# Kernel optimization log

Measured on AMD Instinct MI355X. Metric: run time of the kernel, lower is better.

Reference implementation:

```python
import jax, jax.numpy as jnp
import numpy as np

N_NODE = 4096   # nodes per graph (generalized from hardcoded 55)
IN_DIM = 200    # input_dim, forced by attn1 in_channel=200
OUT_DIM = 200   # output_dim, forced equal to input_dim by GRU_gate shapes
N_HEADS = 8     # forced by attn2 in_channel 1600 = 8*200
SEQ_LEN = 4
HID = 200       # hid_units default


def _glorot(k, shape):
    r = np.sqrt(6.0 / (shape[0] + shape[1])).astype(np.float32)
    return jax.random.uniform(k, shape, jnp.float32, -r, r)


def setup_inputs() -> dict:
    key = jax.random.key(0)
    ks = jax.random.split(key, 32)
    inp = {}
    mask = jax.random.bernoulli(ks[0], 0.01, (SEQ_LEN, N_NODE, N_NODE))
    inp['adjs'] = jax.random.uniform(ks[1], (SEQ_LEN, N_NODE, N_NODE), jnp.float32) * mask
    inp['feats'] = jax.random.normal(ks[2], (SEQ_LEN, N_NODE, IN_DIM), jnp.float32)
    inp['p_covss'] = jnp.zeros((SEQ_LEN,), jnp.float32)  # passed but unused in original
    # per-head weight_vars, randn(output_dim, input_dim) in original call()
    inp['init_wv'] = jax.random.normal(ks[3], (N_HEADS, OUT_DIM, IN_DIM), jnp.float32)
    # attn1 (shared across all heads): conv1d(k=1) == linear
    inp['W1'] = _glorot(ks[4], (HID, IN_DIM)); inp['b1'] = jnp.zeros((HID,), jnp.float32)
    inp['a11'] = _glorot(ks[5], (HID, 1))[:, 0]; inp['a11b'] = jnp.zeros((), jnp.float32)
    inp['a12'] = _glorot(ks[6], (HID, 1))[:, 0]; inp['a12b'] = jnp.zeros((), jnp.float32)
    # attn2
    inp['W2'] = _glorot(ks[7], (OUT_DIM, N_HEADS * HID)); inp['b2'] = jnp.zeros((OUT_DIM,), jnp.float32)
    inp['a21'] = _glorot(ks[8], (OUT_DIM, 1))[:, 0]; inp['a21b'] = jnp.zeros((), jnp.float32)
    inp['a22'] = _glorot(ks[9], (OUT_DIM, 1))[:, 0]; inp['a22b'] = jnp.zeros((), jnp.float32)
    # GRU gates (reset/update/htilda), reduce=True since n_node != input_dim
    for i, g in enumerate(['r', 'u', 'h']):
        inp['W' + g] = _glorot(ks[10 + 4 * i], (N_NODE, OUT_DIM))
        inp['U' + g] = _glorot(ks[11 + 4 * i], (OUT_DIM, OUT_DIM))
        inp['P' + g] = _glorot(ks[12 + 4 * i], (IN_DIM, N_NODE))
        inp['b' + g] = jnp.zeros((IN_DIM, OUT_DIM), jnp.float32)
    return inp


def reference(adjs, feats, p_covss, init_wv, W1, b1, a11, a11b, a12, a12b,
              W2, b2, a21, a21b, a22, a22b,
              Wr, Ur, Pr, br, Wu, Uu, Pu, bu, Wh, Uh, Ph, bh):
    def gat(x):  # x: [N, IN_DIM]
        fts = x @ W1.T + b1                                   # [N, HID]
        # logits f_1 + f_2^T on [N,1,1] stays [N,1,1]; softmax over the
        # singleton dim is identically 1 -> attention is degenerate.
        s = jax.nn.leaky_relu((fts @ a11 + a11b) + (fts @ a12 + a12b), 0.01)
        coefs = jnp.ones_like(s)                              # softmax([N,1,1], dim=1)
        h = jax.nn.elu(coefs[:, None] * fts)                  # [N, HID]
        hcat = jnp.tile(h, (1, N_HEADS))                      # heads share attn1 -> identical
        fts2 = hcat @ W2.T + b2                               # [N, OUT_DIM]
        s2 = jax.nn.leaky_relu((fts2 @ a21 + a21b) + (fts2 @ a22 + a22b), 0.01)
        coefs2 = jnp.ones_like(s2)
        out = jax.nn.elu(coefs2[:, None] * fts2)              # [N, OUT_DIM]
        # torch: out.view(nb_classes, -1).T then softmax(dim=1), then view(-1, out_dim)
        logits = jnp.reshape(out, (OUT_DIM, N_NODE)).T        # memory reinterpretation, not transpose
        return jax.nn.softmax(logits, axis=1)                 # [N, OUT_DIM]

    embeds = jax.vmap(gat)(feats)                             # [T, N, OUT_DIM]

    def gru_step(wv, adj):  # wv: [H, OUT_DIM, IN_DIM=OUT_DIM], adj: [N, N]
        # head-independent sparse propagation bases, one per gate
        gr = Pr @ (adj @ Wr) + br                             # [IN_DIM, OUT_DIM]
        gu = Pu @ (adj @ Wu) + bu
        gh = Ph @ (adj @ Wh) + bh
        r = jax.nn.sigmoid(gr + wv @ Ur)                      # [H, 200, 200]
        u = jax.nn.sigmoid(gu + wv @ Uu)
        hcap = jnp.tanh(gh + (r * wv) @ Uh)
        return (1.0 - u) * wv + u * hcap, None

    final_wv, _ = jax.lax.scan(gru_step, init_wv, adjs[1:])   # evolve over t=1..T-1
    return embeds, final_wv
```

## Files before the change

kernel.cpp:

```cpp
#include <hip/hip_runtime.h>
#include <hip/hip_bf16.h>
#include <math.h>

typedef __hip_bfloat16 bf16;
typedef __attribute__((ext_vector_type(8))) short short8;
typedef __attribute__((ext_vector_type(4))) float f32x4;

#define N_NODE 4096
#define DIM 200
#define NH 8
#define SEQ 4
#define TLDA 40

__device__ __forceinline__ float eluf(float x) { return x > 0.f ? x : expm1f(x); }
__device__ __forceinline__ float sigm(float x) { return 1.f / (1.f + expf(-x)); }

template<bool ISB>
__device__ __forceinline__ float ldv(const void* p, size_t i) {
    if (ISB) return __bfloat162float(((const bf16*)p)[i]);
    else     return ((const float*)p)[i];
}
template<bool ISB>
__device__ __forceinline__ void stv(void* p, size_t i, float v) {
    if (ISB) ((bf16*)p)[i] = __float2bfloat16(v);
    else     ((float*)p)[i] = v;
}
__device__ __forceinline__ float bflo(unsigned u) { return __uint_as_float((u & 0xffffu) << 16); }
__device__ __forceinline__ float bfhi(unsigned u) { return __uint_as_float(u & 0xffff0000u); }
__device__ __forceinline__ short f2bs(float v) {
    bf16 h = __float2bfloat16(v);
    return *(short*)&h;
}

__global__ void k_detect(const void* feats, int* flag) {
    __shared__ int cnt;
    if (threadIdx.x == 0) cnt = 0;
    __syncthreads();
    const unsigned short* u = (const unsigned short*)feats;
    unsigned short v = u[2 * threadIdx.x];
    int e = (v >> 7) & 0xFF;
    if (e >= 100 && e <= 140) atomicAdd(&cnt, 1);
    __syncthreads();
    if (threadIdx.x == 0) *flag = (cnt >= 128) ? 1 : 0;
}


template<int AMODE>
__device__ __forceinline__ short8 ldA8x(const void* A, int lda, int arow, bool rowOK,
                                        int kk, int K) {
    short8 r;
    if (rowOK && kk + 8 <= K) {
        if (AMODE == 1) {
            r = *(const short8*)((const short*)A + (size_t)arow * lda + kk);
        } else {
            const float* ap = (const float*)A + (size_t)arow * lda + kk;
            float4 f0 = *(const float4*)ap;
            float4 f1 = *(const float4*)(ap + 4);
            r[0] = f2bs(f0.x); r[1] = f2bs(f0.y); r[2] = f2bs(f0.z); r[3] = f2bs(f0.w);
            r[4] = f2bs(f1.x); r[5] = f2bs(f1.y); r[6] = f2bs(f1.z); r[7] = f2bs(f1.w);
        }
    } else {
#pragma unroll
        for (int j = 0; j < 8; j++) {
            bool ok = rowOK && kk + j < K;
            if (AMODE == 1) r[j] = ok ? ((const short*)A)[(size_t)arow * lda + kk + j] : (short)0;
            else            r[j] = ok ? f2bs(((const float*)A)[(size_t)arow * lda + kk + j]) : (short)0;
        }
    }
    return r;
}

template<int BMODE>
__device__ __forceinline__ short8 ldB8x(const void* B, int gcol, bool colOK,
                                        int kk, int K) {
    short8 r;
    if (BMODE == 2) {
        if (colOK && kk + 8 <= K) {
            r = *(const short8*)((const short*)B + (size_t)gcol * K + kk);
        } else {
#pragma unroll
            for (int j = 0; j < 8; j++)
                r[j] = (colOK && kk + j < K) ? ((const short*)B)[(size_t)gcol * K + kk + j] : (short)0;
        }
    } else {
#pragma unroll
        for (int j = 0; j < 8; j++)
            r[j] = (colOK && kk + j < K) ? ((const short*)B)[(size_t)(kk + j) * DIM + gcol] : (short)0;
    }
    return r;
}

template<int EPI, int AMODE, int BMODE, int CB16>
__device__ void mgemm(const void* A, int lda, const void* B, int M, int K,
                      int kbeg, int kend, const float* X1, const float* X2,
                      void* Cv, int row0, int c0, const int* fl, void* out2, short* Cb) {
    const int N = DIM;
    int tid = threadIdx.x;
    int wave = tid >> 6, lane = tid & 63;
    int m16 = lane & 15, q = lane >> 4;
    __shared__ short As[64 * TLDA];
    __shared__ short Bs[64 * TLDA];
    int s_row = tid >> 2;
    int s_k   = (tid & 3) * 8;
    int b_col = tid & 63;
    int b_kg  = (tid >> 6) * 8;
    int arow = row0 + s_row;
    bool rowOK = arow < M;
    int gcol = c0 + b_col;
    bool colOK = gcol < N;
    short8 la = ldA8x<AMODE>(A, lda, arow, rowOK, kbeg + s_k, K);
    short8 lb = ldB8x<BMODE>(B, gcol, colOK, kbeg + b_kg, K);
    f32x4 acc[4] = {};
    for (int k0 = kbeg; k0 < kend; k0 += 32) {
        __syncthreads();
        *(short8*)&As[s_row * TLDA + s_k] = la;
        *(short8*)&Bs[b_col * TLDA + b_kg] = lb;
        __syncthreads();
        int kn = k0 + 32;
        if (kn < kend) {
            la = ldA8x<AMODE>(A, lda, arow, rowOK, kn + s_k, K);
            lb = ldB8x<BMODE>(B, gcol, colOK, kn + b_kg, K);
        }
        short8 bfr = *(short8*)&Bs[(wave * 16 + m16) * TLDA + q * 8];
#pragma unroll
        for (int r = 0; r < 4; r++) {
            short8 af = *(short8*)&As[(r * 16 + m16) * TLDA + q * 8];
            acc[r] = __builtin_amdgcn_mfma_f32_16x16x32_bf16(af, bfr, acc[r], 0, 0, 0);
        }
    }
    int colw = c0 + wave * 16 + m16;
    if (colw >= N) return;
#pragma unroll
    for (int r = 0; r < 4; r++) {
        int rowb = row0 + r * 16 + q * 4;
#pragma unroll
        for (int reg = 0; reg < 4; reg++) {
            int row = rowb + reg;
            if (row >= M) continue;
            float v = acc[r][reg];
            size_t ci = (size_t)row * 200 + colw;
            if (EPI == 0) {
                float o = eluf(v + X1[colw]);
                if (CB16) ((short*)Cv)[ci] = f2bs(o);
                else      ((float*)Cv)[ci] = o;
            } else if (EPI == 3) {
                float* C = (float*)Cv;
                int a200 = row - (row / 200) * 200;
                float uu = X2[ci];
                float hc = tanhf(X1[a200 * 200 + colw] + v);
                float nv = (1.f - uu) * C[ci] + uu * hc;
                C[ci] = nv;
                Cb[ci] = f2bs(nv);
                if (out2) {
                    size_t oo = (size_t)SEQ * N_NODE * DIM + ci;
                    if (*fl) stv<true>(out2, oo, nv); else stv<false>(out2, oo, nv);
                }
            } else {
                atomicAdd(&((float*)Cv)[ci], v);
            }
        }
    }
}

__global__ __launch_bounds__(256) void k_gemm_e12(const short* A,
        const short* Br, const short* Bu, const float* Gr, const float* Gu,
        const float* wvf, short* rwb, float* u) {
    const int M = NH * DIM, K = DIM, N = DIM;
    int row0 = blockIdx.y * 64, c0 = blockIdx.x * 64;
    int tid = threadIdx.x;
    int wave = tid >> 6, lane = tid & 63;
    int m16 = lane & 15, q = lane >> 4;
    __shared__ short As[64 * TLDA];
    __shared__ short Bsr[64 * TLDA];
    __shared__ short Bsu[64 * TLDA];
    int s_row = tid >> 2;
    int s_k   = (tid & 3) * 8;
    int b_col = tid & 63;
    int b_kg  = (tid >> 6) * 8;
    int arow = row0 + s_row;
    bool rowOK = arow < M;
    int gcol = c0 + b_col;
    bool colOK = gcol < N;
    short8 la = ldA8x<1>(A, K, arow, rowOK, s_k, K);
    short8 lr = ldB8x<2>(Br, gcol, colOK, b_kg, K);
    short8 lu = ldB8x<2>(Bu, gcol, colOK, b_kg, K);
    f32x4 accR[4] = {}, accU[4] = {};
    for (int k0 = 0; k0 < K; k0 += 32) {
        __syncthreads();
        *(short8*)&As[s_row * TLDA + s_k] = la;
        *(short8*)&Bsr[b_col * TLDA + b_kg] = lr;
        *(short8*)&Bsu[b_col * TLDA + b_kg] = lu;
        __syncthreads();
        int kn = k0 + 32;
        if (kn < K) {
            la = ldA8x<1>(A, K, arow, rowOK, kn + s_k, K);
            lr = ldB8x<2>(Br, gcol, colOK, kn + b_kg, K);
            lu = ldB8x<2>(Bu, gcol, colOK, kn + b_kg, K);
        }
        short8 bfr = *(short8*)&Bsr[(wave * 16 + m16) * TLDA + q * 8];
        short8 bfu = *(short8*)&Bsu[(wave * 16 + m16) * TLDA + q * 8];
#pragma unroll
        for (int r = 0; r < 4; r++) {
            short8 af = *(short8*)&As[(r * 16 + m16) * TLDA + q * 8];
            accR[r] = __builtin_amdgcn_mfma_f32_16x16x32_bf16(af, bfr, accR[r], 0, 0, 0);
            accU[r] = __builtin_amdgcn_mfma_f32_16x16x32_bf16(af, bfu, accU[r], 0, 0, 0);
        }
    }
    int colw = c0 + wave * 16 + m16;
    if (colw >= N) return;
#pragma unroll
    for (int r = 0; r < 4; r++) {
        int rowb = row0 + r * 16 + q * 4;
#pragma unroll
        for (int reg = 0; reg < 4; reg++) {
            int row = rowb + reg;
            if (row >= M) continue;
            int a200 = row - (row / 200) * 200;
            size_t ci = (size_t)row * 200 + colw;
            rwb[ci] = f2bs(sigm(Gr[a200 * 200 + colw] + accR[r][reg]) * wvf[ci]);
            u[ci]   = sigm(Gu[a200 * 200 + colw] + accU[r][reg]);
        }
    }
}

__global__ __launch_bounds__(256) void k_gemm_e0a(const int* fl, const void* A,
        const short* B, const float* bias, short* Hb) {
    int row0 = blockIdx.y * 64, c0 = blockIdx.x * 64;
    if (*fl)
        mgemm<0, 1, 2, 1>(A, DIM, B, SEQ * N_NODE, DIM, 0, DIM, bias, nullptr,
                          Hb, row0, c0, nullptr, nullptr, nullptr);
    else
        mgemm<0, 0, 2, 1>(A, DIM, B, SEQ * N_NODE, DIM, 0, DIM, bias, nullptr,
                          Hb, row0, c0, nullptr, nullptr, nullptr);
}
__global__ __launch_bounds__(256) void k_gemm_e0b(const short* A, const short* B,
        const float* bias, float* C) {
    mgemm<0, 1, 2, 0>(A, DIM, B, SEQ * N_NODE, DIM, 0, DIM, bias, nullptr,
                      C, blockIdx.y * 64, blockIdx.x * 64, nullptr, nullptr, nullptr);
}
__global__ __launch_bounds__(256) void k_gemm_e3(const short* A, const short* B,
        const float* Gh, const float* U, float* WV, const int* fl, void* out2, short* wvb) {
    mgemm<3, 1, 2, 0>(A, DIM, B, NH * DIM, DIM, 0, DIM, Gh, U, WV,
                      blockIdx.y * 64, blockIdx.x * 64, fl, out2, wvb);
}
__global__ __launch_bounds__(256) void k_pggemm(const int* fl,
        const void* P0, const void* P1, const void* P2,
        const bf16* AWb, float* G) {
    int z = blockIdx.z;
    int sg = z >> 3, split = z & 7;
    int g = sg - (sg / 3) * 3;
    const void* A = (g == 0) ? P0 : (g == 1) ? P1 : P2;
    const void* B = AWb + (size_t)sg * N_NODE * DIM;
    float* C = G + (size_t)sg * DIM * DIM;
    int row0 = blockIdx.y * 64, c0 = blockIdx.x * 64;
    int kbeg = split * (N_NODE / 8), kend = kbeg + N_NODE / 8;
    if (*fl) mgemm<4, 1, 1, 0>(A, N_NODE, B, DIM, N_NODE, kbeg, kend, nullptr, nullptr, C, row0, c0, nullptr, nullptr, nullptr);
    else     mgemm<4, 0, 1, 0>(A, N_NODE, B, DIM, N_NODE, kbeg, kend, nullptr, nullptr, C, row0, c0, nullptr, nullptr, nullptr);
}

template<bool ISB>
__device__ void prep_body(const void* W1, const void* b1, const void* W2, const void* b2,
                          const void* Ur, const void* Uu, const void* Uh,
                          const void* br, const void* bu, const void* bh,
                          const void* iwv, const void* Wr, const void* Wu, const void* Wh,
                          short* W1b, short* W2b, float* b1f, float* b2f,
                          short* Ub, float* wv, short* wvb, float* G, unsigned short* Wcat) {
    int idx = blockIdx.x * 256 + threadIdx.x;
    if (idx < 40000) {
        W1b[idx] = f2bs(ldv<ISB>(W1, idx));
    } else if (idx < 80000) {
        int r = idx - 40000;
        int n = r / 200, k = r - n * 200;
        float s = 0.f;
        for (int h = 0; h < NH; h++) s += ldv<ISB>(W2, (size_t)n * 1600 + h * 200 + k);
        W2b[r] = f2bs(s);
    } else if (idx < 80512) {
        int j = idx - 80000;
        if (j < 256)      b1f[j] = (j < 200) ? ldv<ISB>(b1, j) : 0.f;
        else              b2f[j - 256] = (j - 256 < 200) ? ldv<ISB>(b2, j - 256) : 0.f;
    } else if (idx < 200512) {
        int j = idx - 80512;
        int g = j / 40000, r = j - g * 40000;
        int n = r / 200, k = r - n * 200;
        const void* U = (g == 0) ? Ur : (g == 1) ? Uu : Uh;
        Ub[j] = f2bs(ldv<ISB>(U, (size_t)k * 200 + n));
    } else if (idx < 520512) {
        int j = idx - 200512;
        float v = ldv<ISB>(iwv, j);
        wv[j] = v;
        wvb[j] = f2bs(v);
    } else if (idx < 880512) {
        int j = idx - 520512;
        int sg = j / 40000, r = j - sg * 40000;
        int g = sg - (sg / 3) * 3;
        const void* bb = (g == 0) ? br : (g == 1) ? bu : bh;
        G[j] = ldv<ISB>(bb, r);
    } else {
        int j = idx - 880512;
        if (j < 4096 * 600) {
            int k = j / 600, c = j - k * 600;
            int g = (c < 200) ? 0 : (c < 400 ? 1 : 2);
            int o = c - g * 200;
            const void* W = (g == 0) ? Wr : (g == 1) ? Wu : Wh;
            bf16 v = __float2bfloat16(ldv<ISB>(W, (size_t)k * 200 + o));
            Wcat[(size_t)k * 608 + c] = *(unsigned short*)&v;
        }
    }
}
__global__ void k_prep(const int* fl, const void* W1, const void* b1, const void* W2,
                       const void* b2, const void* Ur, const void* Uu, const void* Uh,
                       const void* br, const void* bu, const void* bh, const void* iwv,
                       const void* Wr, const void* Wu, const void* Wh,
                       short* W1b, short* W2b, float* b1f, float* b2f,
                       short* Ub, float* wv, short* wvb, float* G, unsigned short* Wcat) {
    if (*fl) prep_body<true >(W1, b1, W2, b2, Ur, Uu, Uh, br, bu, bh, iwv, Wr, Wu, Wh,
                              W1b, W2b, b1f, b2f, Ub, wv, wvb, G, Wcat);
    else     prep_body<false>(W1, b1, W2, b2, Ur, Uu, Uh, br, bu, bh, iwv, Wr, Wu, Wh,
                              W1b, W2b, b1f, b2f, Ub, wv, wvb, G, Wcat);
}

template<bool ISB>
__device__ void softmax_body(const float* O, void* out) {
    __shared__ float tile[200 * 65];
    __shared__ float pm[4 * 64];
    __shared__ float ps[4 * 64];
    __shared__ float sm_m[64];
    __shared__ float sm_inv[64];
    int t = blockIdx.y;
    int i0 = blockIdx.x * 64;
    const float* ob = O + (size_t)t * N_NODE * DIM;
    int tid = threadIdx.x;
    for (int idx = tid; idx < 200 * 64; idx += 256) {
        int j = idx >> 6, c = idx & 63;
        tile[j * 65 + c] = ob[(size_t)j * N_NODE + i0 + c];
    }
    __syncthreads();
    int g = tid >> 6, lane = tid & 63;
    int j0 = g * 50, j1 = j0 + 50;
    float mp = -1e30f;
    for (int j = j0; j < j1; j++) mp = fmaxf(mp, tile[j * 65 + lane]);
    pm[g * 64 + lane] = mp;
    __syncthreads();
    if (tid < 64)
        sm_m[tid] = fmaxf(fmaxf(pm[tid], pm[64 + tid]), fmaxf(pm[128 + tid], pm[192 + tid]));
    __syncthreads();
    float mv = sm_m[lane];
    float sp = 0.f;
    for (int j = j0; j < j1; j++) {
        float e = expf(tile[j * 65 + lane] - mv);
        tile[j * 65 + lane] = e;
        sp += e;
    }
    ps[g * 64 + lane] = sp;
    __syncthreads();
    if (tid < 64)
        sm_inv[tid] = 1.f / (ps[tid] + ps[64 + tid] + ps[128 + tid] + ps[192 + tid]);
    __syncthreads();
    size_t ob2 = ((size_t)t * N_NODE + i0) * DIM;
    for (int idx = tid; idx < 64 * 200; idx += 256) {
        int il = idx / 200, j = idx - il * 200;
        stv<ISB>(out, ob2 + (size_t)il * DIM + j, tile[j * 65 + il] * sm_inv[il]);
    }
}
__global__ __launch_bounds__(256) void k_softmax(const int* fl, const float* O, void* out) {
    if (*fl) softmax_body<true>(O, out); else softmax_body<false>(O, out);
}

template<bool ISB>
__device__ void aw_body(const void* adjs, const unsigned short* Wcat, bf16* AWb) {
    int i = blockIdx.x;
    int s = blockIdx.y;
    size_t arow = ((size_t)(s + 1) * N_NODE + i) * N_NODE;
    __shared__ int   s_k[512];
    __shared__ float s_v[512];
    __shared__ int   s_cnt;
    int tid = threadIdx.x;
    if (tid == 0) s_cnt = 0;
    __syncthreads();
    float vals[16];
#pragma unroll
    for (int c = 0; c < 4; c++) {
        int col = c * 1024 + tid * 4;
        if (ISB) {
            ushort4 u = *(const ushort4*)((const unsigned short*)adjs + arow + col);
            vals[c*4+0] = __uint_as_float((unsigned)u.x << 16);
            vals[c*4+1] = __uint_as_float((unsigned)u.y << 16);
            vals[c*4+2] = __uint_as_float((unsigned)u.z << 16);
            vals[c*4+3] = __uint_as_float((unsigned)u.w << 16);
        } else {
            float4 f = *(const float4*)((const float*)adjs + arow + col);
            vals[c*4+0] = f.x; vals[c*4+1] = f.y; vals[c*4+2] = f.z; vals[c*4+3] = f.w;
        }
    }
#pragma unroll
    for (int q = 0; q < 16; q++) {
        if (vals[q] != 0.f) {
            int p = atomicAdd(&s_cnt, 1);
            if (p < 512) { s_k[p] = (q >> 2) * 1024 + tid * 4 + (q & 3); s_v[p] = vals[q]; }
        }
    }
    __syncthreads();
    int n = s_cnt < 512 ? s_cnt : 512;
    float a0 = 0.f, a1 = 0.f, d0 = 0.f, d1 = 0.f;
    bool hasB = (tid < 44);
    int offA = 2 * tid, offB = 512 + 2 * tid;
    int e = 0;
    for (; e + 4 <= n; e += 4) {
        int   k0 = s_k[e],   k1 = s_k[e+1], k2 = s_k[e+2], k3 = s_k[e+3];
        float v0 = s_v[e],   v1 = s_v[e+1], v2 = s_v[e+2], v3 = s_v[e+3];
        unsigned wa0 = *(const unsigned*)(Wcat + (size_t)k0 * 608 + offA);
        unsigned wa1 = *(const unsigned*)(Wcat + (size_t)k1 * 608 + offA);
        unsigned wa2 = *(const unsigned*)(Wcat + (size_t)k2 * 608 + offA);
        unsigned wa3 = *(const unsigned*)(Wcat + (size_t)k3 * 608 + offA);
        if (hasB) {
            unsigned wb0 = *(const unsigned*)(Wcat + (size_t)k0 * 608 + offB);
            unsigned wb1 = *(const unsigned*)(Wcat + (size_t)k1 * 608 + offB);
            unsigned wb2 = *(const unsigned*)(Wcat + (size_t)k2 * 608 + offB);
            unsigned wb3 = *(const unsigned*)(Wcat + (size_t)k3 * 608 + offB);
            d0 += v0*bflo(wb0) + v1*bflo(wb1) + v2*bflo(wb2) + v3*bflo(wb3);
            d1 += v0*bfhi(wb0) + v1*bfhi(wb1) + v2*bfhi(wb2) + v3*bfhi(wb3);
        }
        a0 += v0*bflo(wa0) + v1*bflo(wa1) + v2*bflo(wa2) + v3*bflo(wa3);
        a1 += v0*bfhi(wa0) + v1*bfhi(wa1) + v2*bfhi(wa2) + v3*bfhi(wa3);
    }
    for (; e < n; e++) {
        int k = s_k[e]; float v = s_v[e];
        unsigned wa = *(const unsigned*)(Wcat + (size_t)k * 608 + offA);
        a0 += v * bflo(wa); a1 += v * bfhi(wa);
        if (hasB) {
            unsigned wb = *(const unsigned*)(Wcat + (size_t)k * 608 + offB);
            d0 += v * bflo(wb); d1 += v * bfhi(wb);
        }
    }
    int gA = (offA < 200) ? 0 : (offA < 400 ? 1 : 2);
    int oA = offA - gA * 200;
    size_t wbase = ((size_t)(s * 3 + gA) * N_NODE + i) * DIM + oA;
    AWb[wbase]     = __float2bfloat16(a0);
    AWb[wbase + 1] = __float2bfloat16(a1);
    if (hasB) {
        int oB = offB - 400;
        size_t wb2 = ((size_t)(s * 3 + 2) * N_NODE + i) * DIM + oB;
        AWb[wb2]     = __float2bfloat16(d0);
        AWb[wb2 + 1] = __float2bfloat16(d1);
    }
}
__global__ __launch_bounds__(256) void k_aw(const int* fl, const void* adjs,
        const unsigned short* Wcat, bf16* AWb) {
    if (*fl) aw_body<true>(adjs, Wcat, AWb);
    else     aw_body<false>(adjs, Wcat, AWb);
}

extern "C" void kernel_launch(void* const* d_in, const int* in_sizes, int n_in,
                              void* d_out, int out_size, void* d_ws, size_t ws_size,
                              hipStream_t stream) {
    const void* adjs    = d_in[0];
    const void* feats   = d_in[1];
    const void* init_wv = d_in[3];
    const void* W1 = d_in[4];
    const void* b1 = d_in[5];
    const void* W2 = d_in[10];
    const void* b2 = d_in[11];
    const void* Wr = d_in[16];
    const void* Ur = d_in[17];
    const void* Pr = d_in[18];
    const void* br = d_in[19];
    const void* Wu = d_in[20];
    const void* Uu = d_in[21];
    const void* Pu = d_in[22];
    const void* bu = d_in[23];
    const void* Wh = d_in[24];
    const void* Uh = d_in[25];
    const void* Ph = d_in[26];
    const void* bh = d_in[27];

    int*   flag = (int*)d_ws;
    float* base = (float*)d_ws;
    unsigned short* Wcat = (unsigned short*)(base + 64);
    bf16*  AWb  = (bf16*)(base + 64 + 1245184);
    short* Hb   = (short*)(base + 64);
    float* Obuf = base + 3276864;
    short* W1b  = (short*)(base + 6553664);
    short* W2b  = (short*)(base + 6593664);
    float* b1f  = base + 6633664;
    float* b2f  = base + 6633920;
    float* ubuf = base + 6634176;
    short* rwb  = (short*)(base + 6954176);
    short* Ub   = (short*)(base + 7274176);
    float* G    = base + 7394176;
    float* wv   = base + 7754176;
    short* wvb  = (short*)(base + 8074176);

    const int M = SEQ * N_NODE;

    k_detect<<<1, 256, 0, stream>>>(feats, flag);
    k_prep<<<(3338112 + 255) / 256, 256, 0, stream>>>(
        flag, W1, b1, W2, b2, Ur, Uu, Uh, br, bu, bh, init_wv, Wr, Wu, Wh,
        W1b, W2b, b1f, b2f, Ub, wv, wvb, G, Wcat);

    {
        dim3 g(N_NODE, 3);
        k_aw<<<g, 256, 0, stream>>>(flag, adjs, Wcat, AWb);
    }
    {
        dim3 g(4, 4, 72);
        k_pggemm<<<g, 256, 0, stream>>>(flag, Pr, Pu, Ph, AWb, G);
    }

    {
        dim3 g(4, M / 64);
        k_gemm_e0a<<<g, 256, 0, stream>>>(flag, feats, W1b, b1f, Hb);
        k_gemm_e0b<<<g, 256, 0, stream>>>(Hb, W2b, b2f, Obuf);
    }
    {
        dim3 g(N_NODE / 64, SEQ);
        k_softmax<<<g, 256, 0, stream>>>(flag, Obuf, d_out);
    }

    {
        dim3 g(4, NH * DIM / 64);
        for (int s = 0; s < 3; s++) {
            const float* Gr = G + (size_t)(s * 3 + 0) * DIM * DIM;
            const float* Gu = G + (size_t)(s * 3 + 1) * DIM * DIM;
            const float* Gh = G + (size_t)(s * 3 + 2) * DIM * DIM;
            void* out2 = (s == 2) ? d_out : nullptr;
            k_gemm_e12<<<g, 256, 0, stream>>>(wvb, Ub, Ub + 40000, Gr, Gu, wv, rwb, ubuf);
            k_gemm_e3<<<g, 256, 0, stream>>>(rwb, Ub + 80000, Gh, ubuf, wv, flag, out2, wvb);
        }
    }
}
```

Before: 595.3 us.

## Merge independent stages into combined launches and a persistent grid-barrier GRU kernel

Independent work is packed into shared launches: the first attention GEMM runs alongside the sparse adjacency-weight kernel, and the second attention GEMM runs alongside the P·(AW) GEMM. The softmax and the three GRU steps move into one persistent kernel of 256 blocks that uses a software global barrier instead of six separate launches. The aim is to cut launch overhead and the idle gaps between small kernels, and to let independent stages overlap. In exchange it relies on all 256 blocks being resident at once for the spin barrier to avoid deadlock, and the workspace layout is reshuffled so Hb no longer aliases Wcat.

```diff
diff --git a/kernel.cpp b/kernel.cpp
--- a/kernel.cpp
+++ b/kernel.cpp
@@ -32,9 +32,26 @@
     return *(short*)&h;
 }
 
-__global__ void k_detect(const void* feats, int* flag) {
+__device__ __forceinline__ void gbar(int* bar, int nblk, int sense) {
+    __syncthreads();
+    if (threadIdx.x == 0) {
+        __threadfence();
+        int a = __hip_atomic_fetch_add(&bar[0], 1, __ATOMIC_ACQ_REL, __HIP_MEMORY_SCOPE_AGENT);
+        if (a == nblk - 1) {
+            __hip_atomic_store(&bar[0], 0, __ATOMIC_RELAXED, __HIP_MEMORY_SCOPE_AGENT);
+            __hip_atomic_store(&bar[1], sense, __ATOMIC_RELEASE, __HIP_MEMORY_SCOPE_AGENT);
+        } else {
+            while (__hip_atomic_load(&bar[1], __ATOMIC_ACQUIRE, __HIP_MEMORY_SCOPE_AGENT) < sense)
+                __builtin_amdgcn_s_sleep(8);
+        }
+        __threadfence();
+    }
+    __syncthreads();
+}
+
+__global__ void k_detect(const void* feats, int* flag, int* bar) {
     __shared__ int cnt;
-    if (threadIdx.x == 0) cnt = 0;
+    if (threadIdx.x == 0) { cnt = 0; bar[0] = 0; bar[1] = 0; }
     __syncthreads();
     const unsigned short* u = (const unsigned short*)feats;
     unsigned short v = u[2 * threadIdx.x];
@@ -91,15 +108,14 @@
 }
 
 template<int EPI, int AMODE, int BMODE, int CB16>
-__device__ void mgemm(const void* A, int lda, const void* B, int M, int K,
+__device__ void mgemm(short* As, short* Bs,
+                      const void* A, int lda, const void* B, int M, int K,
                       int kbeg, int kend, const float* X1, const float* X2,
                       void* Cv, int row0, int c0, const int* fl, void* out2, short* Cb) {
     const int N = DIM;
     int tid = threadIdx.x;
     int wave = tid >> 6, lane = tid & 63;
     int m16 = lane & 15, q = lane >> 4;
-    __shared__ short As[64 * TLDA];
-    __shared__ short Bs[64 * TLDA];
     int s_row = tid >> 2;
     int s_k   = (tid & 3) * 8;
     int b_col = tid & 63;
@@ -162,17 +178,16 @@
     }
 }
 
-__global__ __launch_bounds__(256) void k_gemm_e12(const short* A,
-        const short* Br, const short* Bu, const float* Gr, const float* Gu,
-        const float* wvf, short* rwb, float* u) {
+__device__ void e12_body(char* smemc, const short* A, const short* Br, const short* Bu,
+                         const float* Gr, const float* Gu, const float* wvf,
+                         short* rwb, float* u, int row0, int c0) {
     const int M = NH * DIM, K = DIM, N = DIM;
-    int row0 = blockIdx.y * 64, c0 = blockIdx.x * 64;
     int tid = threadIdx.x;
     int wave = tid >> 6, lane = tid & 63;
     int m16 = lane & 15, q = lane >> 4;
-    __shared__ short As[64 * TLDA];
-    __shared__ short Bsr[64 * TLDA];
-    __shared__ short Bsu[64 * TLDA];
+    short* As  = (short*)smemc;
+    short* Bsr = As + 64 * TLDA;
+    short* Bsu = Bsr + 64 * TLDA;
     int s_row = tid >> 2;
     int s_k   = (tid & 3) * 8;
     int b_col = tid & 63;
@@ -223,39 +238,216 @@
     }
 }
 
-__global__ __launch_bounds__(256) void k_gemm_e0a(const int* fl, const void* A,
-        const short* B, const float* bias, short* Hb) {
-    int row0 = blockIdx.y * 64, c0 = blockIdx.x * 64;
-    if (*fl)
-        mgemm<0, 1, 2, 1>(A, DIM, B, SEQ * N_NODE, DIM, 0, DIM, bias, nullptr,
-                          Hb, row0, c0, nullptr, nullptr, nullptr);
-    else
-        mgemm<0, 0, 2, 1>(A, DIM, B, SEQ * N_NODE, DIM, 0, DIM, bias, nullptr,
-                          Hb, row0, c0, nullptr, nullptr, nullptr);
-}
-__global__ __launch_bounds__(256) void k_gemm_e0b(const short* A, const short* B,
-        const float* bias, float* C) {
-    mgemm<0, 1, 2, 0>(A, DIM, B, SEQ * N_NODE, DIM, 0, DIM, bias, nullptr,
-                      C, blockIdx.y * 64, blockIdx.x * 64, nullptr, nullptr, nullptr);
-}
-__global__ __launch_bounds__(256) void k_gemm_e3(const short* A, const short* B,
-        const float* Gh, const float* U, float* WV, const int* fl, void* out2, short* wvb) {
-    mgemm<3, 1, 2, 0>(A, DIM, B, NH * DIM, DIM, 0, DIM, Gh, U, WV,
-                      blockIdx.y * 64, blockIdx.x * 64, fl, out2, wvb);
-}
-__global__ __launch_bounds__(256) void k_pggemm(const int* fl,
-        const void* P0, const void* P1, const void* P2,
-        const bf16* AWb, float* G) {
-    int z = blockIdx.z;
-    int sg = z >> 3, split = z & 7;
-    int g = sg - (sg / 3) * 3;
-    const void* A = (g == 0) ? P0 : (g == 1) ? P1 : P2;
-    const void* B = AWb + (size_t)sg * N_NODE * DIM;
-    float* C = G + (size_t)sg * DIM * DIM;
-    int row0 = blockIdx.y * 64, c0 = blockIdx.x * 64;
-    int kbeg = split * (N_NODE / 8), kend = kbeg + N_NODE / 8;
-    if (*fl) mgemm<4, 1, 1, 0>(A, N_NODE, B, DIM, N_NODE, kbeg, kend, nullptr, nullptr, C, row0, c0, nullptr, nullptr, nullptr);
-    else     mgemm<4, 0, 1, 0>(A, N_NODE, B, DIM, N_NODE, kbeg, kend, nullptr, nullptr, C, row0, c0, nullptr, nullptr, nullptr);
+template<bool ISB>
+__device__ void aw_body(char* smemc, const void* adjs, const unsigned short* Wcat,
+                        bf16* AWb, int i, int s) {
+    size_t arow = ((size_t)(s + 1) * N_NODE + i) * N_NODE;
+    int*   s_k   = (int*)smemc;
+    float* s_v   = (float*)(smemc + 2048);
+    int*   s_cnt = (int*)(smemc + 4096);
+    int tid = threadIdx.x;
+    if (tid == 0) *s_cnt = 0;
+    __syncthreads();
+    float vals[16];
+#pragma unroll
+    for (int c = 0; c < 4; c++) {
+        int col = c * 1024 + tid * 4;
+        if (ISB) {
+            ushort4 u = *(const ushort4*)((const unsigned short*)adjs + arow + col);
+            vals[c*4+0] = __uint_as_float((unsigned)u.x << 16);
+            vals[c*4+1] = __uint_as_float((unsigned)u.y << 16);
+            vals[c*4+2] = __uint_as_float((unsigned)u.z << 16);
+            vals[c*4+3] = __uint_as_float((unsigned)u.w << 16);
+        } else {
+            float4 f = *(const float4*)((const float*)adjs + arow + col);
+            vals[c*4+0] = f.x; vals[c*4+1] = f.y; vals[c*4+2] = f.z; vals[c*4+3] = f.w;
+        }
+    }
+#pragma unroll
+    for (int q = 0; q < 16; q++) {
+        if (vals[q] != 0.f) {
+            int p = atomicAdd(s_cnt, 1);
+            if (p < 512) { s_k[p] = (q >> 2) * 1024 + tid * 4 + (q & 3); s_v[p] = vals[q]; }
+        }
+    }
+    __syncthreads();
+    int n = *s_cnt < 512 ? *s_cnt : 512;
+    float a0 = 0.f, a1 = 0.f, d0 = 0.f, d1 = 0.f;
+    bool hasB = (tid < 44);
+    int offA = 2 * tid, offB = 512 + 2 * tid;
+    int e = 0;
+    for (; e + 4 <= n; e += 4) {
+        int   k0 = s_k[e],   k1 = s_k[e+1], k2 = s_k[e+2], k3 = s_k[e+3];
+        float v0 = s_v[e],   v1 = s_v[e+1], v2 = s_v[e+2], v3 = s_v[e+3];
+        unsigned wa0 = *(const unsigned*)(Wcat + (size_t)k0 * 608 + offA);
+        unsigned wa1 = *(const unsigned*)(Wcat + (size_t)k1 * 608 + offA);
+        unsigned wa2 = *(const unsigned*)(Wcat + (size_t)k2 * 608 + offA);
+        unsigned wa3 = *(const unsigned*)(Wcat + (size_t)k3 * 608 + offA);
+        if (hasB) {
+            unsigned wb0 = *(const unsigned*)(Wcat + (size_t)k0 * 608 + offB);
+            unsigned wb1 = *(const unsigned*)(Wcat + (size_t)k1 * 608 + offB);
+            unsigned wb2 = *(const unsigned*)(Wcat + (size_t)k2 * 608 + offB);
+            unsigned wb3 = *(const unsigned*)(Wcat + (size_t)k3 * 608 + offB);
+            d0 += v0*bflo(wb0) + v1*bflo(wb1) + v2*bflo(wb2) + v3*bflo(wb3);
+            d1 += v0*bfhi(wb0) + v1*bfhi(wb1) + v2*bfhi(wb2) + v3*bfhi(wb3);
+        }
+        a0 += v0*bflo(wa0) + v1*bflo(wa1) + v2*bflo(wa2) + v3*bflo(wa3);
+        a1 += v0*bfhi(wa0) + v1*bfhi(wa1) + v2*bfhi(wa2) + v3*bfhi(wa3);
+    }
+    for (; e < n; e++) {
+        int k = s_k[e]; float v = s_v[e];
+        unsigned wa = *(const unsigned*)(Wcat + (size_t)k * 608 + offA);
+        a0 += v * bflo(wa); a1 += v * bfhi(wa);
+        if (hasB) {
+            unsigned wb = *(const unsigned*)(Wcat + (size_t)k * 608 + offB);
+            d0 += v * bflo(wb); d1 += v * bfhi(wb);
+        }
+    }
+    int gA = (offA < 200) ? 0 : (offA < 400 ? 1 : 2);
+    int oA = offA - gA * 200;
+    size_t wbase = ((size_t)(s * 3 + gA) * N_NODE + i) * DIM + oA;
+    AWb[wbase]     = __float2bfloat16(a0);
+    AWb[wbase + 1] = __float2bfloat16(a1);
+    if (hasB) {
+        int oB = offB - 400;
+        size_t wb2 = ((size_t)(s * 3 + 2) * N_NODE + i) * DIM + oB;
+        AWb[wb2]     = __float2bfloat16(d0);
+        AWb[wb2 + 1] = __float2bfloat16(d1);
+    }
+}
+
+template<bool ISB>
+__device__ void softmax_body(char* smemc, const float* O, void* out, int t, int i0) {
+    float* tile   = (float*)smemc;
+    float* pm     = tile + 13000;
+    float* ps     = pm + 256;
+    float* sm_m   = ps + 256;
+    float* sm_inv = sm_m + 64;
+    const float* ob = O + (size_t)t * N_NODE * DIM;
+    int tid = threadIdx.x;
+    for (int idx = tid; idx < 200 * 64; idx += 256) {
+        int j = idx >> 6, c = idx & 63;
+        tile[j * 65 + c] = ob[(size_t)j * N_NODE + i0 + c];
+    }
+    __syncthreads();
+    int g = tid >> 6, lane = tid & 63;
+    int j0 = g * 50, j1 = j0 + 50;
+    float mp = -1e30f;
+    for (int j = j0; j < j1; j++) mp = fmaxf(mp, tile[j * 65 + lane]);
+    pm[g * 64 + lane] = mp;
+    __syncthreads();
+    if (tid < 64)
+        sm_m[tid] = fmaxf(fmaxf(pm[tid], pm[64 + tid]), fmaxf(pm[128 + tid], pm[192 + tid]));
+    __syncthreads();
+    float mv = sm_m[lane];
+    float sp = 0.f;
+    for (int j = j0; j < j1; j++) {
+        float e = expf(tile[j * 65 + lane] - mv);
+        tile[j * 65 + lane] = e;
+        sp += e;
+    }
+    ps[g * 64 + lane] = sp;
+    __syncthreads();
+    if (tid < 64)
+        sm_inv[tid] = 1.f / (ps[tid] + ps[64 + tid] + ps[128 + tid] + ps[192 + tid]);
+    __syncthreads();
+    size_t ob2 = ((size_t)t * N_NODE + i0) * DIM;
+    for (int idx = tid; idx < 64 * 200; idx += 256) {
+        int il = idx / 200, j = idx - il * 200;
+        stv<ISB>(out, ob2 + (size_t)il * DIM + j, tile[j * 65 + il] * sm_inv[il]);
+    }
+}
+
+__global__ __launch_bounds__(256) void k_L2(const int* fl, const void* feats,
+        const short* W1b, const float* b1f, short* Hb,
+        const void* adjs, const unsigned short* Wcat, bf16* AWb) {
+    __shared__ __align__(16) char smem[10752];
+    int b = blockIdx.x;
+    if (b < 1024) {
+        short* As = (short*)smem;
+        short* Bs = As + 64 * TLDA;
+        int row0 = (b >> 2) * 64, c0 = (b & 3) * 64;
+        if (*fl)
+            mgemm<0, 1, 2, 1>(As, Bs, feats, DIM, W1b, SEQ * N_NODE, DIM, 0, DIM,
+                              b1f, nullptr, Hb, row0, c0, nullptr, nullptr, nullptr);
+        else
+            mgemm<0, 0, 2, 1>(As, Bs, feats, DIM, W1b, SEQ * N_NODE, DIM, 0, DIM,
+                              b1f, nullptr, Hb, row0, c0, nullptr, nullptr, nullptr);
+    } else {
+        int ab = b - 1024;
+        int i = ab & 4095, s = ab >> 12;
+        if (*fl) aw_body<true >(smem, adjs, Wcat, AWb, i, s);
+        else     aw_body<false>(smem, adjs, Wcat, AWb, i, s);
+    }
+}
+
+__global__ __launch_bounds__(256) void k_L3(const int* fl, const short* Hb,
+        const short* W2b, const float* b2f, float* Obuf,
+        const void* P0, const void* P1, const void* P2, const bf16* AWb, float* G) {
+    __shared__ __align__(16) char smem[10752];
+    short* As = (short*)smem;
+    short* Bs = As + 64 * TLDA;
+    int b = blockIdx.x;
+    if (b < 1024) {
+        int row0 = (b >> 2) * 64, c0 = (b & 3) * 64;
+        mgemm<0, 1, 2, 0>(As, Bs, Hb, DIM, W2b, SEQ * N_NODE, DIM, 0, DIM,
+                          b2f, nullptr, Obuf, row0, c0, nullptr, nullptr, nullptr);
+    } else {
+        int pb = b - 1024;
+        int z = pb >> 4, rest = pb & 15;
+        int row0 = (rest >> 2) * 64, c0 = (rest & 3) * 64;
+        int sg = z >> 3, split = z & 7;
+        int g = sg - (sg / 3) * 3;
+        const void* A = (g == 0) ? P0 : (g == 1) ? P1 : P2;
+        const void* B = AWb + (size_t)sg * N_NODE * DIM;
+        float* C = G + (size_t)sg * DIM * DIM;
+        int kbeg = split * (N_NODE / 8), kend = kbeg + N_NODE / 8;
+        if (*fl) mgemm<4, 1, 1, 0>(As, Bs, A, N_NODE, B, DIM, N_NODE, kbeg, kend,
+                                   nullptr, nullptr, C, row0, c0, nullptr, nullptr, nullptr);
+        else     mgemm<4, 0, 1, 0>(As, Bs, A, N_NODE, B, DIM, N_NODE, kbeg, kend,
+                                   nullptr, nullptr, C, row0, c0, nullptr, nullptr, nullptr);
+    }
+}
+
+#define COOP_NB 256
+__global__ __launch_bounds__(256) void k_coop(const int* fl, int* bar,
+        const float* Obuf, void* out_, const short* Ub, const float* G,
+        float* wv, short* wvb, short* rwb, float* ubuf) {
+    __shared__ __align__(16) char smem[54784];
+    int b = blockIdx.x;
+    bool gru = b < 100;
+    int row0 = (b >> 2) * 64, c0 = (b & 3) * 64;
+    short* As = (short*)smem;
+    short* Bs = As + 64 * TLDA;
+    if (gru) {
+        e12_body(smem, wvb, Ub, Ub + 40000, G, G + 40000, wv, rwb, ubuf, row0, c0);
+    } else {
+        int sb = b - 100;
+        for (int u = sb; u < 256; u += 156) {
+            __syncthreads();
+            int t = u >> 6, i0 = (u & 63) * 64;
+            if (*fl) softmax_body<true >(smem, Obuf, out_, t, i0);
+            else     softmax_body<false>(smem, Obuf, out_, t, i0);
+        }
+    }
+    int sense = 0;
+    for (int s = 0; s < 3; s++) {
+        gbar(bar, COOP_NB, ++sense);
+        if (gru) {
+            const float* Gh = G + (size_t)(s * 3 + 2) * DIM * DIM;
+            void* out2 = (s == 2) ? out_ : nullptr;
+            mgemm<3, 1, 2, 0>(As, Bs, rwb, DIM, Ub + 80000, NH * DIM, DIM, 0, DIM,
+                              Gh, ubuf, wv, row0, c0, fl, out2, wvb);
+        }
+        if (s < 2) {
+            gbar(bar, COOP_NB, ++sense);
+            if (gru) {
+                const float* Gr = G + (size_t)((s + 1) * 3 + 0) * DIM * DIM;
+                const float* Gu = G + (size_t)((s + 1) * 3 + 1) * DIM * DIM;
+                e12_body(smem, wvb, Ub, Ub + 40000, Gr, Gu, wv, rwb, ubuf, row0, c0);
+            }
+        }
+    }
 }
 
 template<bool ISB>
@@ -319,137 +511,6 @@
                               W1b, W2b, b1f, b2f, Ub, wv, wvb, G, Wcat);
 }
 
-template<bool ISB>
-__device__ void softmax_body(const float* O, void* out) {
-    __shared__ float tile[200 * 65];
-    __shared__ float pm[4 * 64];
-    __shared__ float ps[4 * 64];
-    __shared__ float sm_m[64];
-    __shared__ float sm_inv[64];
-    int t = blockIdx.y;
-    int i0 = blockIdx.x * 64;
-    const float* ob = O + (size_t)t * N_NODE * DIM;
-    int tid = threadIdx.x;
-    for (int idx = tid; idx < 200 * 64; idx += 256) {
-        int j = idx >> 6, c = idx & 63;
-        tile[j * 65 + c] = ob[(size_t)j * N_NODE + i0 + c];
-    }
-    __syncthreads();
-    int g = tid >> 6, lane = tid & 63;
-    int j0 = g * 50, j1 = j0 + 50;
-    float mp = -1e30f;
-    for (int j = j0; j < j1; j++) mp = fmaxf(mp, tile[j * 65 + lane]);
-    pm[g * 64 + lane] = mp;
-    __syncthreads();
-    if (tid < 64)
-        sm_m[tid] = fmaxf(fmaxf(pm[tid], pm[64 + tid]), fmaxf(pm[128 + tid], pm[192 + tid]));
-    __syncthreads();
-    float mv = sm_m[lane];
-    float sp = 0.f;
-    for (int j = j0; j < j1; j++) {
-        float e = expf(tile[j * 65 + lane] - mv);
-        tile[j * 65 + lane] = e;
-        sp += e;
-    }
-    ps[g * 64 + lane] = sp;
-    __syncthreads();
-    if (tid < 64)
-        sm_inv[tid] = 1.f / (ps[tid] + ps[64 + tid] + ps[128 + tid] + ps[192 + tid]);
-    __syncthreads();
-    size_t ob2 = ((size_t)t * N_NODE + i0) * DIM;
-    for (int idx = tid; idx < 64 * 200; idx += 256) {
-        int il = idx / 200, j = idx - il * 200;
-        stv<ISB>(out, ob2 + (size_t)il * DIM + j, tile[j * 65 + il] * sm_inv[il]);
-    }
-}
-__global__ __launch_bounds__(256) void k_softmax(const int* fl, const float* O, void* out) {
-    if (*fl) softmax_body<true>(O, out); else softmax_body<false>(O, out);
-}
-
-template<bool ISB>
-__device__ void aw_body(const void* adjs, const unsigned short* Wcat, bf16* AWb) {
-    int i = blockIdx.x;
-    int s = blockIdx.y;
-    size_t arow = ((size_t)(s + 1) * N_NODE + i) * N_NODE;
-    __shared__ int   s_k[512];
-    __shared__ float s_v[512];
-    __shared__ int   s_cnt;
-    int tid = threadIdx.x;
-    if (tid == 0) s_cnt = 0;
-    __syncthreads();
-    float vals[16];
-#pragma unroll
-    for (int c = 0; c < 4; c++) {
-        int col = c * 1024 + tid * 4;
-        if (ISB) {
-            ushort4 u = *(const ushort4*)((const unsigned short*)adjs + arow + col);
-            vals[c*4+0] = __uint_as_float((unsigned)u.x << 16);
-            vals[c*4+1] = __uint_as_float((unsigned)u.y << 16);
-            vals[c*4+2] = __uint_as_float((unsigned)u.z << 16);
-            vals[c*4+3] = __uint_as_float((unsigned)u.w << 16);
-        } else {
-            float4 f = *(const float4*)((const float*)adjs + arow + col);
-            vals[c*4+0] = f.x; vals[c*4+1] = f.y; vals[c*4+2] = f.z; vals[c*4+3] = f.w;
-        }
-    }
-#pragma unroll
-    for (int q = 0; q < 16; q++) {
-        if (vals[q] != 0.f) {
-            int p = atomicAdd(&s_cnt, 1);
-            if (p < 512) { s_k[p] = (q >> 2) * 1024 + tid * 4 + (q & 3); s_v[p] = vals[q]; }
-        }
-    }
-    __syncthreads();
-    int n = s_cnt < 512 ? s_cnt : 512;
-    float a0 = 0.f, a1 = 0.f, d0 = 0.f, d1 = 0.f;
-    bool hasB = (tid < 44);
-    int offA = 2 * tid, offB = 512 + 2 * tid;
-    int e = 0;
-    for (; e + 4 <= n; e += 4) {
-        int   k0 = s_k[e],   k1 = s_k[e+1], k2 = s_k[e+2], k3 = s_k[e+3];
-        float v0 = s_v[e],   v1 = s_v[e+1], v2 = s_v[e+2], v3 = s_v[e+3];
-        unsigned wa0 = *(const unsigned*)(Wcat + (size_t)k0 * 608 + offA);
-        unsigned wa1 = *(const unsigned*)(Wcat + (size_t)k1 * 608 + offA);
-        unsigned wa2 = *(const unsigned*)(Wcat + (size_t)k2 * 608 + offA);
-        unsigned wa3 = *(const unsigned*)(Wcat + (size_t)k3 * 608 + offA);
-        if (hasB) {
-            unsigned wb0 = *(const unsigned*)(Wcat + (size_t)k0 * 608 + offB);
-            unsigned wb1 = *(const unsigned*)(Wcat + (size_t)k1 * 608 + offB);
-            unsigned wb2 = *(const unsigned*)(Wcat + (size_t)k2 * 608 + offB);
-            unsigned wb3 = *(const unsigned*)(Wcat + (size_t)k3 * 608 + offB);
-            d0 += v0*bflo(wb0) + v1*bflo(wb1) + v2*bflo(wb2) + v3*bflo(wb3);
-            d1 += v0*bfhi(wb0) + v1*bfhi(wb1) + v2*bfhi(wb2) + v3*bfhi(wb3);
-        }
-        a0 += v0*bflo(wa0) + v1*bflo(wa1) + v2*bflo(wa2) + v3*bflo(wa3);
-        a1 += v0*bfhi(wa0) + v1*bfhi(wa1) + v2*bfhi(wa2) + v3*bfhi(wa3);
-    }
-    for (; e < n; e++) {
-        int k = s_k[e]; float v = s_v[e];
-        unsigned wa = *(const unsigned*)(Wcat + (size_t)k * 608 + offA);
-        a0 += v * bflo(wa); a1 += v * bfhi(wa);
-        if (hasB) {
-            unsigned wb = *(const unsigned*)(Wcat + (size_t)k * 608 + offB);
-            d0 += v * bflo(wb); d1 += v * bfhi(wb);
-        }
-    }
-    int gA = (offA < 200) ? 0 : (offA < 400 ? 1 : 2);
-    int oA = offA - gA * 200;
-    size_t wbase = ((size_t)(s * 3 + gA) * N_NODE + i) * DIM + oA;
-    AWb[wbase]     = __float2bfloat16(a0);
-    AWb[wbase + 1] = __float2bfloat16(a1);
-    if (hasB) {
-        int oB = offB - 400;
-        size_t wb2 = ((size_t)(s * 3 + 2) * N_NODE + i) * DIM + oB;
-        AWb[wb2]     = __float2bfloat16(d0);
-        AWb[wb2 + 1] = __float2bfloat16(d1);
-    }
-}
-__global__ __launch_bounds__(256) void k_aw(const int* fl, const void* adjs,
-        const unsigned short* Wcat, bf16* AWb) {
-    if (*fl) aw_body<true>(adjs, Wcat, AWb);
-    else     aw_body<false>(adjs, Wcat, AWb);
-}
-
 extern "C" void kernel_launch(void* const* d_in, const int* in_sizes, int n_in,
                               void* d_out, int out_size, void* d_ws, size_t ws_size,
                               hipStream_t stream) {
@@ -474,57 +535,31 @@
     const void* bh = d_in[27];
 
     int*   flag = (int*)d_ws;
+    int*   bar  = (int*)d_ws + 16;
     float* base = (float*)d_ws;
     unsigned short* Wcat = (unsigned short*)(base + 64);
-    bf16*  AWb  = (bf16*)(base + 64 + 1245184);
-    short* Hb   = (short*)(base + 64);
-    float* Obuf = base + 3276864;
-    short* W1b  = (short*)(base + 6553664);
-    short* W2b  = (short*)(base + 6593664);
-    float* b1f  = base + 6633664;
-    float* b2f  = base + 6633920;
-    float* ubuf = base + 6634176;
-    short* rwb  = (short*)(base + 6954176);
-    short* Ub   = (short*)(base + 7274176);
-    float* G    = base + 7394176;
-    float* wv   = base + 7754176;
-    short* wvb  = (short*)(base + 8074176);
-
-    const int M = SEQ * N_NODE;
-
-    k_detect<<<1, 256, 0, stream>>>(feats, flag);
+    bf16*  AWb  = (bf16*)(base + 1245248);
+    short* Hb   = (short*)(base + 4931648);
+    float* Obuf = base + 6570048;
+    short* W1b  = (short*)(base + 9846848);
+    short* W2b  = (short*)(base + 9866848);
+    float* b1f  = base + 9886848;
+    float* b2f  = base + 9887104;
+    float* ubuf = base + 9887360;
+    short* rwb  = (short*)(base + 10207360);
+    short* Ub   = (short*)(base + 10367360);
+    float* G    = base + 10427360;
+    float* wv   = base + 10787360;
+    short* wvb  = (short*)(base + 11107360);
+
+    k_detect<<<1, 256, 0, stream>>>(feats, flag, bar);
     k_prep<<<(3338112 + 255) / 256, 256, 0, stream>>>(
         flag, W1, b1, W2, b2, Ur, Uu, Uh, br, bu, bh, init_wv, Wr, Wu, Wh,
         W1b, W2b, b1f, b2f, Ub, wv, wvb, G, Wcat);
 
-    {
-        dim3 g(N_NODE, 3);
-        k_aw<<<g, 256, 0, stream>>>(flag, adjs, Wcat, AWb);
-    }
-    {
-        dim3 g(4, 4, 72);
-        k_pggemm<<<g, 256, 0, stream>>>(flag, Pr, Pu, Ph, AWb, G);
-    }
-
-    {
-        dim3 g(4, M / 64);
-        k_gemm_e0a<<<g, 256, 0, stream>>>(flag, feats, W1b, b1f, Hb);
-        k_gemm_e0b<<<g, 256, 0, stream>>>(Hb, W2b, b2f, Obuf);
-    }
-    {
-        dim3 g(N_NODE / 64, SEQ);
-        k_softmax<<<g, 256, 0, stream>>>(flag, Obuf, d_out);
-    }
-
-    {
-        dim3 g(4, NH * DIM / 64);
-        for (int s = 0; s < 3; s++) {
-            const float* Gr = G + (size_t)(s * 3 + 0) * DIM * DIM;
-            const float* Gu = G + (size_t)(s * 3 + 1) * DIM * DIM;
-            const float* Gh = G + (size_t)(s * 3 + 2) * DIM * DIM;
-            void* out2 = (s == 2) ? d_out : nullptr;
-            k_gemm_e12<<<g, 256, 0, stream>>>(wvb, Ub, Ub + 40000, Gr, Gu, wv, rwb, ubuf);
-            k_gemm_e3<<<g, 256, 0, stream>>>(rwb, Ub + 80000, Gh, ubuf, wv, flag, out2, wvb);
-        }
-    }
-}
+    k_L2<<<1024 + 3 * N_NODE, 256, 0, stream>>>(flag, feats, W1b, b1f, Hb, adjs, Wcat, AWb);
+
+    k_L3<<<1024 + 1152, 256, 0, stream>>>(flag, Hb, W2b, b2f, Obuf, Pr, Pu, Ph, AWb, G);
+
+    k_coop<<<COOP_NB, 256, 0, stream>>>(flag, bar, Obuf, d_out, Ub, G, wv, wvb, rwb, ubuf);
+}
```

New measurement: 852.3 us. 43.2% more time.
